# Optimization experiments

Measured on AMD Instinct MI355X. Metric: run time of the kernel, lower is better.

The kernel has to match this reference:

```python
import jax, jax.numpy as jnp
import numpy as np

B, S, D = 1, 2048, 2048
H = 16
HD = D // H           # 128
FFN_H = 5632          # int(2*4*D/3) rounded up to multiple of 256
EPS = 1e-5
ROPE_THETA = 10000.0


def rms_norm(x, w, eps=EPS):
    # x * rsqrt(mean(x^2, -1) + eps) * w
    return x * jax.lax.rsqrt(jnp.mean(x * x, axis=-1, keepdims=True) + eps) * w


def apply_rope(x, cos, sin):
    # x: [B, S, H, HD]; cos/sin: [S, HD//2]
    b, s, h, hd = x.shape
    xr = x.reshape(b, s, h, hd // 2, 2)
    x_re, x_im = xr[..., 0], xr[..., 1]
    c = cos[None, :, None, :]
    sn = sin[None, :, None, :]
    o_re = x_re * c - x_im * sn
    o_im = x_re * sn + x_im * c
    return jnp.stack([o_re, o_im], axis=-1).reshape(b, s, h, hd)


def setup_inputs() -> dict:
    key = jax.random.key(0)
    ks = jax.random.split(key, 10)
    x = jax.random.normal(ks[0], (B, S, D), dtype=jnp.float32)
    # RoPE frequencies (Llama-style)
    inv_freq = 1.0 / (ROPE_THETA ** (np.arange(0, HD, 2, dtype=np.float32) / HD))
    angles = np.outer(np.arange(S, dtype=np.float32), inv_freq)  # [S, HD//2]
    freqs_cos = jnp.asarray(np.cos(angles), dtype=jnp.float32)
    freqs_sin = jnp.asarray(np.sin(angles), dtype=jnp.float32)
    # causal mask: 1 = keep, 0 = masked
    mask = jnp.tril(jnp.ones((S, S), dtype=jnp.int32))[None, None]
    sc = 0.02
    return {
        "x": x,
        "freqs_cos": freqs_cos,
        "freqs_sin": freqs_sin,
        "mask": mask,
        "wq": jax.random.normal(ks[1], (D, D), jnp.float32) * sc,
        "wk": jax.random.normal(ks[2], (D, D), jnp.float32) * sc,
        "wv": jax.random.normal(ks[3], (D, D), jnp.float32) * sc,
        "wo": jax.random.normal(ks[4], (D, D), jnp.float32) * sc,
        "w1": jax.random.normal(ks[5], (D, FFN_H), jnp.float32) * sc,
        "w2": jax.random.normal(ks[6], (FFN_H, D), jnp.float32) * sc,
        "w3": jax.random.normal(ks[7], (D, FFN_H), jnp.float32) * sc,
        "attn_norm_w": jnp.ones((D,), jnp.float32),
        "ffn_norm_w": jnp.ones((D,), jnp.float32),
    }


def reference(x, freqs_cos, freqs_sin, mask, wq, wk, wv, wo, w1, w2, w3,
              attn_norm_w, ffn_norm_w):
    b, s, d = x.shape
    # --- attention block ---
    xn = rms_norm(x, attn_norm_w)
    q = (xn @ wq).reshape(b, s, H, HD)
    k = (xn @ wk).reshape(b, s, H, HD)
    v = (xn @ wv).reshape(b, s, H, HD)
    q = apply_rope(q, freqs_cos, freqs_sin)
    k = apply_rope(k, freqs_cos, freqs_sin)
    scores = jnp.einsum('bqhd,bkhd->bhqk', q, k) / jnp.sqrt(jnp.float32(HD))
    scores = jnp.where(mask == 0, -jnp.inf, scores)
    probs = jax.nn.softmax(scores, axis=-1)
    attn = jnp.einsum('bhqk,bkhd->bqhd', probs, v).reshape(b, s, d)
    h = x + attn @ wo
    # --- SwiGLU FFN block ---
    hn = rms_norm(h, ffn_norm_w)
    ff = (jax.nn.silu(hn @ w1) * (hn @ w3)) @ w2
    return h + ff
```

## Files before the change

### kernel.cpp

```cpp
#include <hip/hip_runtime.h>
#include <hip/hip_bf16.h>

typedef __bf16 bf16x8 __attribute__((ext_vector_type(8)));
typedef float f32x4 __attribute__((ext_vector_type(4)));
typedef unsigned short u16x8 __attribute__((ext_vector_type(8)));
typedef unsigned short u16x4 __attribute__((ext_vector_type(4)));

#define DEV static __device__ __forceinline__

DEV unsigned short f2bf(float f) {
    unsigned u = __builtin_bit_cast(unsigned, f);
    u += 0x7fffu + ((u >> 16) & 1u);
    return (unsigned short)(u >> 16);
}
DEV float bf2f(unsigned short h) {
    unsigned u = ((unsigned)h) << 16;
    return __builtin_bit_cast(float, u);
}

DEV void gl2lds16(const void* g, void* l) {
    __builtin_amdgcn_global_load_lds(
        (const __attribute__((address_space(1))) void*)g,
        (__attribute__((address_space(3))) void*)l, 16, 0, 0);
}

#define STAGE256(KT, SLOT, BUF)                                               \
    {                                                                         \
        const unsigned short* sbase = ((SLOT) & 1)                            \
            ? BT + (size_t)(bn + ((SLOT) >> 1) * 128) * K                     \
            : A  + (size_t)(bm + ((SLOT) >> 1) * 128) * K;                    \
        _Pragma("unroll")                                                     \
        for (int j = 0; j < 2; ++j) {                                         \
            const unsigned short* g = sbase + (size_t)(srow + j * 64) * K     \
                                      + (KT) * 64 + lc;                       \
            gl2lds16(g, &lds[BUF][SLOT][wave * 512 + j * 4096]);              \
        }                                                                     \
    }

#define COMPUTE256(BUF, MH, NH)                                               \
    {                                                                         \
        const char* Ab = (const char*)&lds[BUF][(MH) * 2][0];                 \
        const char* Bb = (const char*)&lds[BUF][(NH) * 2 + 1][0];             \
        bf16x8 a_[4][2], b_[2][2];                                            \
        _Pragma("unroll")                                                     \
        for (int m4 = 0; m4 < 4; ++m4) {                                      \
            _Pragma("unroll")                                                 \
            for (int kk = 0; kk < 2; ++kk)                                    \
                a_[m4][kk] = *(const bf16x8*)(Ab +                            \
                    (wm * 64 + m4 * 16 + lr) * 128 +                          \
                    ((kk * 64 + lg * 16) ^ xsw));                             \
        }                                                                     \
        _Pragma("unroll")                                                     \
        for (int n2 = 0; n2 < 2; ++n2) {                                      \
            _Pragma("unroll")                                                 \
            for (int kk = 0; kk < 2; ++kk)                                    \
                b_[n2][kk] = *(const bf16x8*)(Bb +                            \
                    (wn * 32 + n2 * 16 + lr) * 128 +                          \
                    ((kk * 64 + lg * 16) ^ xsw));                             \
        }                                                                     \
        __builtin_amdgcn_s_setprio(1);                                        \
        _Pragma("unroll")                                                     \
        for (int m4 = 0; m4 < 4; ++m4)                                        \
            _Pragma("unroll")                                                 \
            for (int n2 = 0; n2 < 2; ++n2)                                    \
                _Pragma("unroll")                                             \
                for (int kk = 0; kk < 2; ++kk)                                \
                    acc[(MH) * 4 + m4][(NH) * 2 + n2] =                       \
                        __builtin_amdgcn_mfma_f32_16x16x32_bf16(              \
                            a_[m4][kk], b_[n2][kk],                           \
                            acc[(MH) * 4 + m4][(NH) * 2 + n2], 0, 0, 0);      \
        __builtin_amdgcn_s_setprio(0);                                        \
    }

#define WAITV(N) asm volatile("s_waitcnt vmcnt(" #N ")" ::: "memory")
#define SBAR()   asm volatile("s_barrier" ::: "memory")

__global__ __launch_bounds__(512, 2)
void gemm256_bt(const unsigned short* __restrict__ A,
                const unsigned short* __restrict__ BT,
                unsigned short* __restrict__ outB,
                int M, int N, int K)
{
    __shared__ alignas(16) unsigned short lds[2][4][8192];

    const int tid  = threadIdx.x;
    const int lane = tid & 63;
    const int wave = tid >> 6;
    const int wm = wave >> 2;
    const int wn = wave & 3;
    const int lr = lane & 15;
    const int lg = lane >> 4;
    const int bm = blockIdx.y * 256;
    const int bn = blockIdx.x * 256;
    const int xsw  = (lr & 7) << 4;
    const int srow = tid >> 3;
    const int lc   = ((tid & 7) ^ (srow & 7)) * 8;

    f32x4 acc[8][4] = {};

    const int NT = K >> 6;

    STAGE256(0, 0, 0); STAGE256(0, 1, 0); STAGE256(0, 2, 0); STAGE256(0, 3, 0);

    for (int kt = 0; kt < NT - 1; ++kt) {
        const int buf = kt & 1, nbuf = buf ^ 1;
        STAGE256(kt + 1, 0, nbuf);
        WAITV(6); SBAR();
        COMPUTE256(buf, 0, 0);
        STAGE256(kt + 1, 1, nbuf);
        WAITV(6); SBAR();
        COMPUTE256(buf, 1, 0);
        STAGE256(kt + 1, 2, nbuf);
        WAITV(6); SBAR();
        COMPUTE256(buf, 1, 1);
        STAGE256(kt + 1, 3, nbuf);
        COMPUTE256(buf, 0, 1);
        SBAR();
    }
    {
        const int buf = (NT - 1) & 1;
        WAITV(4); SBAR();
        COMPUTE256(buf, 0, 0);
        WAITV(2); SBAR();
        COMPUTE256(buf, 1, 0);
        WAITV(0); SBAR();
        COMPUTE256(buf, 1, 1);
        COMPUTE256(buf, 0, 1);
    }

#pragma unroll
    for (int m = 0; m < 8; ++m) {
        const int row = bm + (m >> 2) * 128 + wm * 64 + (m & 3) * 16 + lg * 4;
#pragma unroll
        for (int n = 0; n < 4; ++n) {
            const int col = bn + (n >> 1) * 128 + wn * 32 + (n & 1) * 16 + lr;
#pragma unroll
            for (int r = 0; r < 4; ++r)
                outB[(size_t)(row + r) * N + col] = f2bf(acc[m][n][r]);
        }
    }
}

template <int EPI, int BM>
__global__ __launch_bounds__(256)
void gemm_bt(const unsigned short* __restrict__ A,
             const unsigned short* __restrict__ BT,
             unsigned short* __restrict__ outB,
             float* __restrict__ outF,
             const float* __restrict__ res,
             int M, int N, int K)
{
    constexpr int AM = BM / 32;
    constexpr int CAW = BM / 64;
    __shared__ alignas(16) unsigned short As[BM][32];
    __shared__ alignas(16) unsigned short Bs[128][32];

    const int tid  = threadIdx.x;
    const int lane = tid & 63;
    const int wave = tid >> 6;
    const int bm = blockIdx.y * BM;
    const int bn = blockIdx.x * 128;
    const int wm = (wave >> 1) * (BM / 2);
    const int wn = (wave & 1) * 64;
    const int lr = lane & 15;
    const int lg = lane >> 4;
    const int sub = lane >> 2;
    const int cb  = (lane & 3) * 16;

    f32x4 acc[AM][4] = {};

    auto stage = [&](int kt) {
#pragma unroll
        for (int ch = 0; ch < CAW; ++ch) {
            const int rb = wave * (CAW * 16) + ch * 16;
            const void* g = (const char*)(A + (size_t)(bm + rb + sub) * K + kt * 32) + cb;
            gl2lds16(g, &As[rb][0]);
        }
#pragma unroll
        for (int ch = 0; ch < 2; ++ch) {
            const int rb = wave * 32 + ch * 16;
            const void* g = (const char*)(BT + (size_t)(bn + rb + sub) * K + kt * 32) + cb;
            gl2lds16(g, &Bs[rb][0]);
        }
    };

    const int NT = K >> 5;
    for (int kt = 0; kt < NT; ++kt) {
        stage(kt);
        __syncthreads();
        bf16x8 af[AM], bfr[4];
#pragma unroll
        for (int i = 0; i < AM; ++i)
            af[i] = *reinterpret_cast<const bf16x8*>(&As[wm + i * 16 + lr][lg * 8]);
#pragma unroll
        for (int j = 0; j < 4; ++j)
            bfr[j] = *reinterpret_cast<const bf16x8*>(&Bs[wn + j * 16 + lr][lg * 8]);
#pragma unroll
        for (int i = 0; i < AM; ++i)
#pragma unroll
            for (int j = 0; j < 4; ++j)
                acc[i][j] = __builtin_amdgcn_mfma_f32_16x16x32_bf16(af[i], bfr[j], acc[i][j], 0, 0, 0);
        __syncthreads();
    }

#pragma unroll
    for (int i = 0; i < AM; ++i) {
#pragma unroll
        for (int j = 0; j < 4; ++j) {
            const int col = bn + wn + j * 16 + lr;
#pragma unroll
            for (int r = 0; r < 4; ++r) {
                const int row = bm + wm + i * 16 + lg * 4 + r;
                const float v = acc[i][j][r];
                if constexpr (EPI == 0) {
                    outB[(size_t)row * N + col] = f2bf(v);
                } else {
                    outF[(size_t)row * N + col] = res[(size_t)row * N + col] + v;
                }
            }
        }
    }
}

__global__ __launch_bounds__(256)
void rmsnorm_kernel(const float* __restrict__ x, const float* __restrict__ w,
                    unsigned short* __restrict__ out)
{
    const int row = blockIdx.x;
    const int tid = threadIdx.x;
    const float* xr = x + (size_t)row * 2048;
    const float4 a = *reinterpret_cast<const float4*>(xr + tid * 8);
    const float4 b = *reinterpret_cast<const float4*>(xr + tid * 8 + 4);
    float ss = a.x * a.x + a.y * a.y + a.z * a.z + a.w * a.w
             + b.x * b.x + b.y * b.y + b.z * b.z + b.w * b.w;
#pragma unroll
    for (int off = 32; off; off >>= 1) ss += __shfl_xor(ss, off);
    __shared__ float red[4];
    if ((tid & 63) == 0) red[tid >> 6] = ss;
    __syncthreads();
    const float tot = red[0] + red[1] + red[2] + red[3];
    const float sc = rsqrtf(tot * (1.0f / 2048.0f) + 1e-5f);
    const float4 wa = *reinterpret_cast<const float4*>(w + tid * 8);
    const float4 wb = *reinterpret_cast<const float4*>(w + tid * 8 + 4);
    u16x8 o;
    o[0] = f2bf(a.x * sc * wa.x); o[1] = f2bf(a.y * sc * wa.y);
    o[2] = f2bf(a.z * sc * wa.z); o[3] = f2bf(a.w * sc * wa.w);
    o[4] = f2bf(b.x * sc * wb.x); o[5] = f2bf(b.y * sc * wb.y);
    o[6] = f2bf(b.z * sc * wb.z); o[7] = f2bf(b.w * sc * wb.w);
    *reinterpret_cast<u16x8*>(out + (size_t)row * 2048 + tid * 8) = o;
}

__global__ __launch_bounds__(256)
void rope_kernel(unsigned short* __restrict__ t, const float* __restrict__ cs,
                 const float* __restrict__ sn)
{
    const int idx = blockIdx.x * 256 + threadIdx.x;
    const int s   = idx >> 9;
    const int col = (idx & 511) * 8;
    const int i0  = (col & 127) >> 1;
    u16x8 v = *reinterpret_cast<const u16x8*>(t + (size_t)s * 6144 + col);
    const float4 c  = *reinterpret_cast<const float4*>(cs + s * 64 + i0);
    const float4 sv = *reinterpret_cast<const float4*>(sn + s * 64 + i0);
    const float cc[4] = {c.x, c.y, c.z, c.w};
    const float ns[4] = {sv.x, sv.y, sv.z, sv.w};
#pragma unroll
    for (int p = 0; p < 4; ++p) {
        const float re = bf2f(v[2 * p]), im = bf2f(v[2 * p + 1]);
        v[2 * p]     = f2bf(re * cc[p] - im * ns[p]);
        v[2 * p + 1] = f2bf(re * ns[p] + im * cc[p]);
    }
    *reinterpret_cast<u16x8*>(t + (size_t)s * 6144 + col) = v;
}

__global__ __launch_bounds__(256)
void transpose_bf16(const unsigned short* __restrict__ in,
                    unsigned short* __restrict__ out, int M, int N, int ldin)
{
    __shared__ unsigned short t[64][66];
    const int bm = blockIdx.y * 64, bn = blockIdx.x * 64;
    const int tid = threadIdx.x;
    const int r = tid >> 3, c8 = (tid & 7) * 8;
#pragma unroll
    for (int i = 0; i < 2; ++i) {
        const int row = r + i * 32;
        u16x8 v = *reinterpret_cast<const u16x8*>(in + (size_t)(bm + row) * ldin + bn + c8);
#pragma unroll
        for (int e = 0; e < 8; ++e) t[row][c8 + e] = v[e];
    }
    __syncthreads();
#pragma unroll
    for (int i = 0; i < 2; ++i) {
        const int orow = r + i * 32;
        u16x8 v;
#pragma unroll
        for (int e = 0; e < 8; ++e) v[e] = t[c8 + e][orow];
        *reinterpret_cast<u16x8*>(out + (size_t)(bn + orow) * M + bm + c8) = v;
    }
}

__global__ __launch_bounds__(256)
void convT_kernel(const float* __restrict__ w, unsigned short* __restrict__ wT,
                  int K, int N)
{
    __shared__ unsigned short t[64][66];
    const int bk = blockIdx.y * 64, bn = blockIdx.x * 64;
    const int tid = threadIdx.x;
    const int r = tid >> 4, c4 = (tid & 15) * 4;
#pragma unroll
    for (int i = 0; i < 4; ++i) {
        const int row = r + i * 16;
        const float4 v = *reinterpret_cast<const float4*>(w + (size_t)(bk + row) * N + bn + c4);
        t[row][c4 + 0] = f2bf(v.x); t[row][c4 + 1] = f2bf(v.y);
        t[row][c4 + 2] = f2bf(v.z); t[row][c4 + 3] = f2bf(v.w);
    }
    __syncthreads();
#pragma unroll
    for (int i = 0; i < 4; ++i) {
        const int n = r + i * 16;
        u16x4 o;
#pragma unroll
        for (int e = 0; e < 4; ++e) o[e] = t[c4 + e][n];
        *reinterpret_cast<u16x4*>(wT + (size_t)(bn + n) * K + bk + c4) = o;
    }
}

__global__ __launch_bounds__(256)
void silu_mul_kernel(const unsigned short* __restrict__ t13,
                     unsigned short* __restrict__ g)
{
    const int s  = blockIdx.y;
    const int c8 = (blockIdx.x * 256 + threadIdx.x) * 8;
    if (c8 >= 5632) return;
    const unsigned short* row = t13 + (size_t)s * 11264;
    const u16x8 va = *reinterpret_cast<const u16x8*>(row + c8);
    const u16x8 vb = *reinterpret_cast<const u16x8*>(row + 5632 + c8);
    u16x8 o;
#pragma unroll
    for (int e = 0; e < 8; ++e) {
        const float x = bf2f(va[e]);
        const float y = bf2f(vb[e]);
        const float sv = x / (1.0f + __expf(-x));
        o[e] = f2bf(sv * y);
    }
    *reinterpret_cast<u16x8*>(g + (size_t)s * 5632 + c8) = o;
}

__global__ __launch_bounds__(512)
void flash_attn(const unsigned short* __restrict__ q,
                const unsigned short* __restrict__ k,
                const unsigned short* __restrict__ vT,
                unsigned short* __restrict__ attn)
{
    __shared__ alignas(16) unsigned short Ks[2][64][136];
    __shared__ alignas(16) unsigned short Vs[2][128][72];
    __shared__ alignas(16) unsigned short Ps[8][16][72];

    const int hh = blockIdx.y;
    const int pi = blockIdx.x;
    const int tid = threadIdx.x;
    const int lane = tid & 63, wave = tid >> 6;
    const int qt = (wave >> 2) ? (31 - pi) : pi;
    const int lr = lane & 15, lg = lane >> 4;
    const int q0 = qt * 64 + (wave & 3) * 16;
    const int myNT = qt + 1;
    const int NT   = 32 - pi;

    const int kr0 = tid >> 4, kc0 = (tid & 15) * 8;
    const int vr0 = tid >> 3, vc0 = (tid & 7) * 8;

    bf16x8 qf[4];
#pragma unroll
    for (int c = 0; c < 4; ++c)
        qf[c] = *reinterpret_cast<const bf16x8*>(
            q + (size_t)(q0 + lr) * 6144 + hh * 128 + c * 32 + lg * 8);

    f32x4 oacc[8] = {};
    float m_r[4], l_r[4];
#pragma unroll
    for (int r = 0; r < 4; ++r) { m_r[r] = -INFINITY; l_r[r] = 0.0f; }
    const float scale = 0.08838834764831845f;

    u16x8 kreg0, kreg1, vreg0, vreg1;
    auto gload = [&](int kt) {
        const int kv0 = kt * 64;
        kreg0 = *reinterpret_cast<const u16x8*>(k + (size_t)(kv0 + kr0) * 6144 + hh * 128 + kc0);
        kreg1 = *reinterpret_cast<const u16x8*>(k + (size_t)(kv0 + kr0 + 32) * 6144 + hh * 128 + kc0);
        vreg0 = *reinterpret_cast<const u16x8*>(vT + (size_t)(hh * 128 + vr0) * 2048 + kv0 + vc0);
        vreg1 = *reinterpret_cast<const u16x8*>(vT + (size_t)(hh * 128 + vr0 + 64) * 2048 + kv0 + vc0);
    };
    auto lwrite = [&](int buf) {
        *reinterpret_cast<u16x8*>(&Ks[buf][kr0][kc0])      = kreg0;
        *reinterpret_cast<u16x8*>(&Ks[buf][kr0 + 32][kc0]) = kreg1;
        *reinterpret_cast<u16x8*>(&Vs[buf][vr0][vc0])      = vreg0;
        *reinterpret_cast<u16x8*>(&Vs[buf][vr0 + 64][vc0]) = vreg1;
    };

    gload(0); lwrite(0);
    __syncthreads();

    for (int kt = 0; kt < NT; ++kt) {
        const int buf = kt & 1;
        if (kt + 1 < NT) gload(kt + 1);

        if (kt < myNT) {
            const int kv0 = kt * 64;
            const bool masked = (kt == myNT - 1);
            f32x4 s[4] = {};
            __builtin_amdgcn_s_setprio(1);
#pragma unroll
            for (int ct = 0; ct < 4; ++ct)
#pragma unroll
                for (int c = 0; c < 4; ++c) {
                    const bf16x8 kf = *reinterpret_cast<const bf16x8*>(
                        &Ks[buf][ct * 16 + lr][c * 32 + lg * 8]);
                    s[ct] = __builtin_amdgcn_mfma_f32_16x16x32_bf16(qf[c], kf, s[ct], 0, 0, 0);
                }
            __builtin_amdgcn_s_setprio(0);
#pragma unroll
            for (int ct = 0; ct < 4; ++ct)
#pragma unroll
                for (int r = 0; r < 4; ++r) {
                    float v = s[ct][r] * scale;
                    if (masked) {
                        const int kvg = kv0 + ct * 16 + lr;
                        const int qg  = q0 + lg * 4 + r;
                        if (kvg > qg) v = -INFINITY;
                    }
                    s[ct][r] = v;
                }
            float mn[4], alpha[4], rs[4];
#pragma unroll
            for (int r = 0; r < 4; ++r) {
                float v = fmaxf(fmaxf(s[0][r], s[1][r]), fmaxf(s[2][r], s[3][r]));
                v = fmaxf(v, __shfl_xor(v, 1));
                v = fmaxf(v, __shfl_xor(v, 2));
                v = fmaxf(v, __shfl_xor(v, 4));
                v = fmaxf(v, __shfl_xor(v, 8));
                mn[r] = fmaxf(m_r[r], v);
                alpha[r] = __expf(m_r[r] - mn[r]);
                m_r[r] = mn[r];
                rs[r] = 0.0f;
            }
#pragma unroll
            for (int ct = 0; ct < 4; ++ct)
#pragma unroll
                for (int r = 0; r < 4; ++r) {
                    const float p = __expf(s[ct][r] - mn[r]);
                    s[ct][r] = p;
                    rs[r] += p;
                }
#pragma unroll
            for (int r = 0; r < 4; ++r) {
                float t2 = rs[r];
                t2 += __shfl_xor(t2, 1);
                t2 += __shfl_xor(t2, 2);
                t2 += __shfl_xor(t2, 4);
                t2 += __shfl_xor(t2, 8);
                l_r[r] = l_r[r] * alpha[r] + t2;
            }
#pragma unroll
            for (int ot = 0; ot < 8; ++ot)
#pragma unroll
                for (int r = 0; r < 4; ++r) oacc[ot][r] *= alpha[r];

#pragma unroll
            for (int ct = 0; ct < 4; ++ct)
#pragma unroll
                for (int r = 0; r < 4; ++r)
                    Ps[wave][lg * 4 + r][ct * 16 + lr] = f2bf(s[ct][r]);

            __builtin_amdgcn_s_setprio(1);
#pragma unroll
            for (int c2 = 0; c2 < 2; ++c2) {
                const bf16x8 pf = *reinterpret_cast<const bf16x8*>(
                    &Ps[wave][lr][c2 * 32 + lg * 8]);
#pragma unroll
                for (int ot = 0; ot < 8; ++ot) {
                    const bf16x8 vf = *reinterpret_cast<const bf16x8*>(
                        &Vs[buf][ot * 16 + lr][c2 * 32 + lg * 8]);
                    oacc[ot] = __builtin_amdgcn_mfma_f32_16x16x32_bf16(pf, vf, oacc[ot], 0, 0, 0);
                }
            }
            __builtin_amdgcn_s_setprio(0);
        }

        if (kt + 1 < NT) lwrite(buf ^ 1);
        __syncthreads();
    }

#pragma unroll
    for (int ot = 0; ot < 8; ++ot)
#pragma unroll
        for (int r = 0; r < 4; ++r) {
            const float v = oacc[ot][r] / l_r[r];
            attn[(size_t)(q0 + lg * 4 + r) * 2048 + hh * 128 + ot * 16 + lr] = f2bf(v);
        }
}

extern "C" void kernel_launch(void* const* d_in, const int* in_sizes, int n_in,
                              void* d_out, int out_size, void* d_ws, size_t ws_size,
                              hipStream_t stream)
{
    const float* x    = (const float*)d_in[0];
    const float* fcos = (const float*)d_in[1];
    const float* fsin = (const float*)d_in[2];
    const float* wq  = (const float*)d_in[4];
    const float* wk  = (const float*)d_in[5];
    const float* wv  = (const float*)d_in[6];
    const float* wo  = (const float*)d_in[7];
    const float* w1  = (const float*)d_in[8];
    const float* w2  = (const float*)d_in[9];
    const float* w3  = (const float*)d_in[10];
    const float* anw = (const float*)d_in[11];
    const float* fnw = (const float*)d_in[12];
    float* out = (float*)d_out;

    char* ws = (char*)d_ws;
    size_t off = 0;
    auto alloc = [&](size_t bytes) { void* p = ws + off; off += bytes; return p; };
    const size_t SZ_DD = (size_t)2048 * 2048 * 2;
    const size_t SZ_DF = (size_t)2048 * 5632 * 2;

    unsigned short* wqT = (unsigned short*)alloc(SZ_DD);
    unsigned short* wkT = (unsigned short*)alloc(SZ_DD);
    unsigned short* wvT = (unsigned short*)alloc(SZ_DD);
    unsigned short* woT = (unsigned short*)alloc(SZ_DD);
    unsigned short* w1T = (unsigned short*)alloc(SZ_DF);
    unsigned short* w3T = (unsigned short*)alloc(SZ_DF);
    unsigned short* w2T = (unsigned short*)alloc(SZ_DF);

    char* reg1 = (char*)alloc((size_t)48 * 1024 * 1024);
    unsigned short* xn   = (unsigned short*)reg1;
    unsigned short* qkv  = (unsigned short*)(reg1 + SZ_DD);
    unsigned short* vTb  = (unsigned short*)(reg1 + SZ_DD + 3 * SZ_DD);
    unsigned short* ab   = (unsigned short*)(reg1 + SZ_DD + 4 * SZ_DD);
    unsigned short* t13  = (unsigned short*)reg1;

    char* reg2 = (char*)alloc(SZ_DF);
    unsigned short* hn = (unsigned short*)reg2;
    unsigned short* t1 = (unsigned short*)reg2;

    convT_kernel<<<dim3(32, 32), 256, 0, stream>>>(wq, wqT, 2048, 2048);
    convT_kernel<<<dim3(32, 32), 256, 0, stream>>>(wk, wkT, 2048, 2048);
    convT_kernel<<<dim3(32, 32), 256, 0, stream>>>(wv, wvT, 2048, 2048);
    convT_kernel<<<dim3(32, 32), 256, 0, stream>>>(wo, woT, 2048, 2048);
    convT_kernel<<<dim3(88, 32), 256, 0, stream>>>(w1, w1T, 2048, 5632);
    convT_kernel<<<dim3(88, 32), 256, 0, stream>>>(w3, w3T, 2048, 5632);
    convT_kernel<<<dim3(32, 88), 256, 0, stream>>>(w2, w2T, 5632, 2048);

    rmsnorm_kernel<<<2048, 256, 0, stream>>>(x, anw, xn);
    gemm256_bt<<<dim3(24, 8), 512, 0, stream>>>(xn, wqT, qkv, 2048, 6144, 2048);
    rope_kernel<<<4096, 256, 0, stream>>>(qkv, fcos, fsin);
    transpose_bf16<<<dim3(32, 32), 256, 0, stream>>>(qkv + 4096, vTb, 2048, 2048, 6144);
    flash_attn<<<dim3(16, 16), 512, 0, stream>>>(qkv, qkv + 2048, vTb, ab);
    gemm_bt<1, 64><<<dim3(16, 32), 256, 0, stream>>>(ab, woT, nullptr, out, x, 2048, 2048, 2048);

    rmsnorm_kernel<<<2048, 256, 0, stream>>>(out, fnw, hn);
    gemm256_bt<<<dim3(44, 8), 512, 0, stream>>>(hn, w1T, t13, 2048, 11264, 2048);
    silu_mul_kernel<<<dim3(3, 2048), 256, 0, stream>>>(t13, t1);
    gemm_bt<1, 64><<<dim3(16, 32), 256, 0, stream>>>(t1, w2T, nullptr, out, out, 2048, 2048, 5632);
}
```

Before: 488.3 us.

## Use pipelined 256-tile split-K GEMM for output projections and swizzle tile order

The simple 64x128 GEMM used for the wo and w2 projections is replaced by the double-buffered 256x256 GEMM, split over K into two halves. Each half writes fp32 partials, and a separate kernel sums them with the residual. All 256-tile GEMMs also remap block indices so that consecutive blocks share column tiles, which is meant to improve L2 reuse. The cost is extra fp32 partial traffic and a reduce launch. The split-K grid is only 128 blocks, which may underfill the GPU.

Measured after the change: 474.5 us. -2.8%, faster.

```diff
diff --git a/kernel.cpp b/kernel.cpp
--- a/kernel.cpp
+++ b/kernel.cpp
@@ -32,7 +32,7 @@
         _Pragma("unroll")                                                     \
         for (int j = 0; j < 2; ++j) {                                         \
             const unsigned short* g = sbase + (size_t)(srow + j * 64) * K     \
-                                      + (KT) * 64 + lc;                       \
+                                      + koff + (KT) * 64 + lc;                \
             gl2lds16(g, &lds[BUF][SLOT][wave * 512 + j * 4096]);              \
         }                                                                     \
     }
@@ -75,6 +75,51 @@
 #define WAITV(N) asm volatile("s_waitcnt vmcnt(" #N ")" ::: "memory")
 #define SBAR()   asm volatile("s_barrier" ::: "memory")
 
+#define GEMM256_PREAMBLE                                                      \
+    const int tid  = threadIdx.x;                                             \
+    const int lane = tid & 63;                                                \
+    const int wave = tid >> 6;                                                \
+    const int wm = wave >> 2;                                                 \
+    const int wn = wave & 3;                                                  \
+    const int lr = lane & 15;                                                 \
+    const int lg = lane >> 4;                                                 \
+    const int lin = blockIdx.y * gridDim.x + blockIdx.x;                      \
+    const int cpx = (gridDim.x * gridDim.y) >> 3;                             \
+    const int swz = (lin & 7) * cpx + (lin >> 3);                             \
+    const int bm = (swz & 7) * 256;            \
+    const int bn = (swz >> 3) * 256;                                          \
+    const int xsw  = (lr & 7) << 4;                                           \
+    const int srow = tid >> 3;                                                \
+    const int lc   = ((tid & 7) ^ (srow & 7)) * 8;
+
+#define GEMM256_MAINLOOP                                                      \
+    STAGE256(0, 0, 0); STAGE256(0, 1, 0); STAGE256(0, 2, 0); STAGE256(0, 3, 0);\
+    for (int kt = 0; kt < NT - 1; ++kt) {                                     \
+        const int buf = kt & 1, nbuf = buf ^ 1;                               \
+        STAGE256(kt + 1, 0, nbuf);                                            \
+        WAITV(6); SBAR();                                                     \
+        COMPUTE256(buf, 0, 0);                                                \
+        STAGE256(kt + 1, 1, nbuf);                                            \
+        WAITV(6); SBAR();                                                     \
+        COMPUTE256(buf, 1, 0);                                                \
+        STAGE256(kt + 1, 2, nbuf);                                            \
+        WAITV(6); SBAR();                                                     \
+        COMPUTE256(buf, 1, 1);                                                \
+        STAGE256(kt + 1, 3, nbuf);                                            \
+        COMPUTE256(buf, 0, 1);                                                \
+        SBAR();                                                               \
+    }                                                                         \
+    {                                                                         \
+        const int buf = (NT - 1) & 1;                                         \
+        WAITV(4); SBAR();                                                     \
+        COMPUTE256(buf, 0, 0);                                                \
+        WAITV(2); SBAR();                                                     \
+        COMPUTE256(buf, 1, 0);                                                \
+        WAITV(0); SBAR();                                                     \
+        COMPUTE256(buf, 1, 1);                                                \
+        COMPUTE256(buf, 0, 1);                                                \
+    }
+
 __global__ __launch_bounds__(512, 2)
 void gemm256_bt(const unsigned short* __restrict__ A,
                 const unsigned short* __restrict__ BT,
@@ -82,51 +127,12 @@
                 int M, int N, int K)
 {
     __shared__ alignas(16) unsigned short lds[2][4][8192];
-
-    const int tid  = threadIdx.x;
-    const int lane = tid & 63;
-    const int wave = tid >> 6;
-    const int wm = wave >> 2;
-    const int wn = wave & 3;
-    const int lr = lane & 15;
-    const int lg = lane >> 4;
-    const int bm = blockIdx.y * 256;
-    const int bn = blockIdx.x * 256;
-    const int xsw  = (lr & 7) << 4;
-    const int srow = tid >> 3;
-    const int lc   = ((tid & 7) ^ (srow & 7)) * 8;
-
+    GEMM256_PREAMBLE
+    const int koff = 0;
     f32x4 acc[8][4] = {};
-
     const int NT = K >> 6;
 
-    STAGE256(0, 0, 0); STAGE256(0, 1, 0); STAGE256(0, 2, 0); STAGE256(0, 3, 0);
-
-    for (int kt = 0; kt < NT - 1; ++kt) {
-        const int buf = kt & 1, nbuf = buf ^ 1;
-        STAGE256(kt + 1, 0, nbuf);
-        WAITV(6); SBAR();
-        COMPUTE256(buf, 0, 0);
-        STAGE256(kt + 1, 1, nbuf);
-        WAITV(6); SBAR();
-        COMPUTE256(buf, 1, 0);
-        STAGE256(kt + 1, 2, nbuf);
-        WAITV(6); SBAR();
-        COMPUTE256(buf, 1, 1);
-        STAGE256(kt + 1, 3, nbuf);
-        COMPUTE256(buf, 0, 1);
-        SBAR();
-    }
-    {
-        const int buf = (NT - 1) & 1;
-        WAITV(4); SBAR();
-        COMPUTE256(buf, 0, 0);
-        WAITV(2); SBAR();
-        COMPUTE256(buf, 1, 0);
-        WAITV(0); SBAR();
-        COMPUTE256(buf, 1, 1);
-        COMPUTE256(buf, 0, 1);
-    }
+    GEMM256_MAINLOOP
 
 #pragma unroll
     for (int m = 0; m < 8; ++m) {
@@ -141,84 +147,46 @@
     }
 }
 
-template <int EPI, int BM>
+__global__ __launch_bounds__(512, 2)
+void gemm256_splitk(const unsigned short* __restrict__ A,
+                    const unsigned short* __restrict__ BT,
+                    float* __restrict__ outP,
+                    int M, int N, int K)
+{
+    __shared__ alignas(16) unsigned short lds[2][4][8192];
+    GEMM256_PREAMBLE
+    const int Kh = K >> 1;
+    const int koff = blockIdx.z * Kh;
+    f32x4 acc[8][4] = {};
+    const int NT = Kh >> 6;
+
+    GEMM256_MAINLOOP
+
+    float* P = outP + (size_t)blockIdx.z * M * N;
+#pragma unroll
+    for (int m = 0; m < 8; ++m) {
+        const int row = bm + (m >> 2) * 128 + wm * 64 + (m & 3) * 16 + lg * 4;
+#pragma unroll
+        for (int n = 0; n < 4; ++n) {
+            const int col = bn + (n >> 1) * 128 + wn * 32 + (n & 1) * 16 + lr;
+#pragma unroll
+            for (int r = 0; r < 4; ++r)
+                P[(size_t)(row + r) * N + col] = acc[m][n][r];
+        }
+    }
+}
+
 __global__ __launch_bounds__(256)
-void gemm_bt(const unsigned short* __restrict__ A,
-             const unsigned short* __restrict__ BT,
-             unsigned short* __restrict__ outB,
-             float* __restrict__ outF,
-             const float* __restrict__ res,
-             int M, int N, int K)
-{
-    constexpr int AM = BM / 32;
-    constexpr int CAW = BM / 64;
-    __shared__ alignas(16) unsigned short As[BM][32];
-    __shared__ alignas(16) unsigned short Bs[128][32];
-
-    const int tid  = threadIdx.x;
-    const int lane = tid & 63;
-    const int wave = tid >> 6;
-    const int bm = blockIdx.y * BM;
-    const int bn = blockIdx.x * 128;
-    const int wm = (wave >> 1) * (BM / 2);
-    const int wn = (wave & 1) * 64;
-    const int lr = lane & 15;
-    const int lg = lane >> 4;
-    const int sub = lane >> 2;
-    const int cb  = (lane & 3) * 16;
-
-    f32x4 acc[AM][4] = {};
-
-    auto stage = [&](int kt) {
-#pragma unroll
-        for (int ch = 0; ch < CAW; ++ch) {
-            const int rb = wave * (CAW * 16) + ch * 16;
-            const void* g = (const char*)(A + (size_t)(bm + rb + sub) * K + kt * 32) + cb;
-            gl2lds16(g, &As[rb][0]);
-        }
-#pragma unroll
-        for (int ch = 0; ch < 2; ++ch) {
-            const int rb = wave * 32 + ch * 16;
-            const void* g = (const char*)(BT + (size_t)(bn + rb + sub) * K + kt * 32) + cb;
-            gl2lds16(g, &Bs[rb][0]);
-        }
-    };
-
-    const int NT = K >> 5;
-    for (int kt = 0; kt < NT; ++kt) {
-        stage(kt);
-        __syncthreads();
-        bf16x8 af[AM], bfr[4];
-#pragma unroll
-        for (int i = 0; i < AM; ++i)
-            af[i] = *reinterpret_cast<const bf16x8*>(&As[wm + i * 16 + lr][lg * 8]);
-#pragma unroll
-        for (int j = 0; j < 4; ++j)
-            bfr[j] = *reinterpret_cast<const bf16x8*>(&Bs[wn + j * 16 + lr][lg * 8]);
-#pragma unroll
-        for (int i = 0; i < AM; ++i)
-#pragma unroll
-            for (int j = 0; j < 4; ++j)
-                acc[i][j] = __builtin_amdgcn_mfma_f32_16x16x32_bf16(af[i], bfr[j], acc[i][j], 0, 0, 0);
-        __syncthreads();
-    }
-
-#pragma unroll
-    for (int i = 0; i < AM; ++i) {
-#pragma unroll
-        for (int j = 0; j < 4; ++j) {
-            const int col = bn + wn + j * 16 + lr;
-#pragma unroll
-            for (int r = 0; r < 4; ++r) {
-                const int row = bm + wm + i * 16 + lg * 4 + r;
-                const float v = acc[i][j][r];
-                if constexpr (EPI == 0) {
-                    outB[(size_t)row * N + col] = f2bf(v);
-                } else {
-                    outF[(size_t)row * N + col] = res[(size_t)row * N + col] + v;
-                }
-            }
-        }
+void reduce2_add(const float* res, const float* p, float* out, int n4)
+{
+    const float4* r4 = (const float4*)res;
+    const float4* a4 = (const float4*)p;
+    const float4* b4 = (const float4*)(p + (size_t)2048 * 2048);
+    float4* o4 = (float4*)out;
+    for (int i = blockIdx.x * 256 + threadIdx.x; i < n4; i += gridDim.x * 256) {
+        const float4 r = r4[i], a = a4[i], b = b4[i];
+        o4[i] = make_float4(r.x + a.x + b.x, r.y + a.y + b.y,
+                            r.z + a.z + b.z, r.w + a.w + b.w);
     }
 }
 
@@ -535,10 +503,13 @@
     unsigned short* vTb  = (unsigned short*)(reg1 + SZ_DD + 3 * SZ_DD);
     unsigned short* ab   = (unsigned short*)(reg1 + SZ_DD + 4 * SZ_DD);
     unsigned short* t13  = (unsigned short*)reg1;
+    float*          pk   = (float*)reg1;
 
     char* reg2 = (char*)alloc(SZ_DF);
     unsigned short* hn = (unsigned short*)reg2;
     unsigned short* t1 = (unsigned short*)reg2;
+
+    const int N4 = 2048 * 2048 / 4;
 
     convT_kernel<<<dim3(32, 32), 256, 0, stream>>>(wq, wqT, 2048, 2048);
     convT_kernel<<<dim3(32, 32), 256, 0, stream>>>(wk, wkT, 2048, 2048);
@@ -553,10 +524,12 @@
     rope_kernel<<<4096, 256, 0, stream>>>(qkv, fcos, fsin);
     transpose_bf16<<<dim3(32, 32), 256, 0, stream>>>(qkv + 4096, vTb, 2048, 2048, 6144);
     flash_attn<<<dim3(16, 16), 512, 0, stream>>>(qkv, qkv + 2048, vTb, ab);
-    gemm_bt<1, 64><<<dim3(16, 32), 256, 0, stream>>>(ab, woT, nullptr, out, x, 2048, 2048, 2048);
+    gemm256_splitk<<<dim3(8, 8, 2), 512, 0, stream>>>(ab, woT, pk, 2048, 2048, 2048);
+    reduce2_add<<<2048, 256, 0, stream>>>(x, pk, out, N4);
 
     rmsnorm_kernel<<<2048, 256, 0, stream>>>(out, fnw, hn);
     gemm256_bt<<<dim3(44, 8), 512, 0, stream>>>(hn, w1T, t13, 2048, 11264, 2048);
     silu_mul_kernel<<<dim3(3, 2048), 256, 0, stream>>>(t13, t1);
-    gemm_bt<1, 64><<<dim3(16, 32), 256, 0, stream>>>(t1, w2T, nullptr, out, out, 2048, 2048, 5632);
-}
+    gemm256_splitk<<<dim3(8, 8, 2), 512, 0, stream>>>(t1, w2T, pk, 2048, 2048, 5632);
+    reduce2_add<<<2048, 256, 0, stream>>>(out, pk, out, N4);
+}
```

## Replace small GEMMs with split-K 128x256 kernel, fuse reduce with RMSNorm, swizzle blocks

Applied to the files above, without the earlier changes.

Drops the simple single-buffered gemm_bt kernel and adds a double-buffered 128x256 LDS-staged GEMM. The Wo and W2 projections use it in split-K form (two halves written as fp32 partials), followed by a reduction kernel. For Wo, the reduction also adds the residual and performs the FFN RMSNorm, which removes a separate norm pass. The W1/W3 GEMM moves to the 128-row tile to get more blocks. Block-index swizzling is added to both GEMMs for L2 locality. In exchange, the split-K path writes and re-reads fp32 partial buffers through global memory.

Result: faster. 450.6 us (-7.7%).

```diff
diff --git a/kernel.cpp b/kernel.cpp
--- a/kernel.cpp
+++ b/kernel.cpp
@@ -23,6 +23,9 @@
         (const __attribute__((address_space(1))) void*)g,
         (__attribute__((address_space(3))) void*)l, 16, 0, 0);
 }
+
+#define WAITV(N) asm volatile("s_waitcnt vmcnt(" #N ")" ::: "memory")
+#define SBAR()   asm volatile("s_barrier" ::: "memory")
 
 #define STAGE256(KT, SLOT, BUF)                                               \
     {                                                                         \
@@ -72,9 +75,6 @@
         __builtin_amdgcn_s_setprio(0);                                        \
     }
 
-#define WAITV(N) asm volatile("s_waitcnt vmcnt(" #N ")" ::: "memory")
-#define SBAR()   asm volatile("s_barrier" ::: "memory")
-
 __global__ __launch_bounds__(512, 2)
 void gemm256_bt(const unsigned short* __restrict__ A,
                 const unsigned short* __restrict__ BT,
@@ -82,7 +82,6 @@
                 int M, int N, int K)
 {
     __shared__ alignas(16) unsigned short lds[2][4][8192];
-
     const int tid  = threadIdx.x;
     const int lane = tid & 63;
     const int wave = tid >> 6;
@@ -90,18 +89,19 @@
     const int wn = wave & 3;
     const int lr = lane & 15;
     const int lg = lane >> 4;
-    const int bm = blockIdx.y * 256;
-    const int bn = blockIdx.x * 256;
+    const int lin = blockIdx.y * gridDim.x + blockIdx.x;
+    const int cpx = (gridDim.x * gridDim.y) >> 3;
+    const int swz = (lin & 7) * cpx + (lin >> 3);
+    const int bm = (swz & 7) * 256;
+    const int bn = (swz >> 3) * 256;
     const int xsw  = (lr & 7) << 4;
     const int srow = tid >> 3;
     const int lc   = ((tid & 7) ^ (srow & 7)) * 8;
 
     f32x4 acc[8][4] = {};
-
     const int NT = K >> 6;
 
     STAGE256(0, 0, 0); STAGE256(0, 1, 0); STAGE256(0, 2, 0); STAGE256(0, 3, 0);
-
     for (int kt = 0; kt < NT - 1; ++kt) {
         const int buf = kt & 1, nbuf = buf ^ 1;
         STAGE256(kt + 1, 0, nbuf);
@@ -141,84 +141,159 @@
     }
 }
 
-template <int EPI, int BM>
-__global__ __launch_bounds__(256)
-void gemm_bt(const unsigned short* __restrict__ A,
-             const unsigned short* __restrict__ BT,
-             unsigned short* __restrict__ outB,
-             float* __restrict__ outF,
-             const float* __restrict__ res,
-             int M, int N, int K)
-{
-    constexpr int AM = BM / 32;
-    constexpr int CAW = BM / 64;
-    __shared__ alignas(16) unsigned short As[BM][32];
-    __shared__ alignas(16) unsigned short Bs[128][32];
-
+#define STAGE128(KT, SLOT, BUF)                                               \
+    {                                                                         \
+        const unsigned short* sbase = ((SLOT) == 0)                           \
+            ? A  + (size_t)bm * K                                             \
+            : BT + (size_t)(bn + ((SLOT) - 1) * 128) * K;                     \
+        _Pragma("unroll")                                                     \
+        for (int j = 0; j < 2; ++j) {                                         \
+            const unsigned short* g = sbase + (size_t)(srow + j * 64) * K     \
+                                      + koff + (KT) * 64 + lc;                \
+            gl2lds16(g, &lds[BUF][SLOT][wave * 512 + j * 4096]);              \
+        }                                                                     \
+    }
+
+#define COMPUTE128(BUF, KK)                                                   \
+    {                                                                         \
+        const char* Ab = (const char*)&lds[BUF][0][0];                        \
+        const char* Bb = (const char*)&lds[BUF][1 + (wn >> 1)][0];            \
+        bf16x8 a_[4], b_[4];                                                  \
+        _Pragma("unroll")                                                     \
+        for (int m4 = 0; m4 < 4; ++m4)                                        \
+            a_[m4] = *(const bf16x8*)(Ab + (wm * 64 + m4 * 16 + lr) * 128 +   \
+                     (((KK) * 64 + lg * 16) ^ xsw));                          \
+        _Pragma("unroll")                                                     \
+        for (int n2 = 0; n2 < 4; ++n2)                                        \
+            b_[n2] = *(const bf16x8*)(Bb +                                    \
+                     ((wn & 1) * 64 + n2 * 16 + lr) * 128 +                   \
+                     (((KK) * 64 + lg * 16) ^ xsw));                          \
+        __builtin_amdgcn_s_setprio(1);                                        \
+        _Pragma("unroll")                                                     \
+        for (int m4 = 0; m4 < 4; ++m4)                                        \
+            _Pragma("unroll")                                                 \
+            for (int n2 = 0; n2 < 4; ++n2)                                    \
+                acc[m4][n2] = __builtin_amdgcn_mfma_f32_16x16x32_bf16(        \
+                    a_[m4], b_[n2], acc[m4][n2], 0, 0, 0);                    \
+        __builtin_amdgcn_s_setprio(0);                                        \
+    }
+
+template <bool SPLITK>
+__global__ __launch_bounds__(512, 2)
+void gemm128_bt(const unsigned short* __restrict__ A,
+                const unsigned short* __restrict__ BT,
+                unsigned short* __restrict__ outB,
+                float* __restrict__ outP,
+                int M, int N, int K)
+{
+    __shared__ alignas(16) unsigned short lds[2][3][8192];
     const int tid  = threadIdx.x;
     const int lane = tid & 63;
     const int wave = tid >> 6;
-    const int bm = blockIdx.y * BM;
-    const int bn = blockIdx.x * 128;
-    const int wm = (wave >> 1) * (BM / 2);
-    const int wn = (wave & 1) * 64;
+    const int wm = wave >> 2;
+    const int wn = wave & 3;
     const int lr = lane & 15;
     const int lg = lane >> 4;
-    const int sub = lane >> 2;
-    const int cb  = (lane & 3) * 16;
-
-    f32x4 acc[AM][4] = {};
-
-    auto stage = [&](int kt) {
-#pragma unroll
-        for (int ch = 0; ch < CAW; ++ch) {
-            const int rb = wave * (CAW * 16) + ch * 16;
-            const void* g = (const char*)(A + (size_t)(bm + rb + sub) * K + kt * 32) + cb;
-            gl2lds16(g, &As[rb][0]);
-        }
-#pragma unroll
-        for (int ch = 0; ch < 2; ++ch) {
-            const int rb = wave * 32 + ch * 16;
-            const void* g = (const char*)(BT + (size_t)(bn + rb + sub) * K + kt * 32) + cb;
-            gl2lds16(g, &Bs[rb][0]);
-        }
-    };
-
-    const int NT = K >> 5;
-    for (int kt = 0; kt < NT; ++kt) {
-        stage(kt);
-        __syncthreads();
-        bf16x8 af[AM], bfr[4];
-#pragma unroll
-        for (int i = 0; i < AM; ++i)
-            af[i] = *reinterpret_cast<const bf16x8*>(&As[wm + i * 16 + lr][lg * 8]);
-#pragma unroll
-        for (int j = 0; j < 4; ++j)
-            bfr[j] = *reinterpret_cast<const bf16x8*>(&Bs[wn + j * 16 + lr][lg * 8]);
-#pragma unroll
-        for (int i = 0; i < AM; ++i)
-#pragma unroll
-            for (int j = 0; j < 4; ++j)
-                acc[i][j] = __builtin_amdgcn_mfma_f32_16x16x32_bf16(af[i], bfr[j], acc[i][j], 0, 0, 0);
-        __syncthreads();
-    }
-
-#pragma unroll
-    for (int i = 0; i < AM; ++i) {
-#pragma unroll
-        for (int j = 0; j < 4; ++j) {
-            const int col = bn + wn + j * 16 + lr;
+    const int gy  = gridDim.y;
+    const int lin = blockIdx.y * gridDim.x + blockIdx.x;
+    const int cpx = (gridDim.x * gy) >> 3;
+    const int swz = (lin & 7) * cpx + (lin >> 3);
+    const int bm = (swz % gy) * 128;
+    const int bn = (swz / gy) * 256;
+    const int xsw  = (lr & 7) << 4;
+    const int srow = tid >> 3;
+    const int lc   = ((tid & 7) ^ (srow & 7)) * 8;
+    int koff, NT;
+    if constexpr (SPLITK) { const int Kh = K >> 1; koff = blockIdx.z * Kh; NT = Kh >> 6; }
+    else                  { koff = 0;              NT = K >> 6; }
+
+    f32x4 acc[4][4] = {};
+
+    STAGE128(0, 0, 0); STAGE128(0, 1, 0); STAGE128(0, 2, 0);
+    for (int kt = 0; kt < NT - 1; ++kt) {
+        const int buf = kt & 1, nbuf = buf ^ 1;
+        STAGE128(kt + 1, 0, nbuf);
+        STAGE128(kt + 1, 1, nbuf);
+        WAITV(4); SBAR();
+        COMPUTE128(buf, 0);
+        STAGE128(kt + 1, 2, nbuf);
+        COMPUTE128(buf, 1);
+        SBAR();
+    }
+    {
+        const int buf = (NT - 1) & 1;
+        WAITV(0); SBAR();
+        COMPUTE128(buf, 0);
+        COMPUTE128(buf, 1);
+    }
+
+#pragma unroll
+    for (int m4 = 0; m4 < 4; ++m4) {
+        const int row = bm + wm * 64 + m4 * 16 + lg * 4;
+#pragma unroll
+        for (int n2 = 0; n2 < 4; ++n2) {
+            const int col = bn + wn * 64 + n2 * 16 + lr;
 #pragma unroll
             for (int r = 0; r < 4; ++r) {
-                const int row = bm + wm + i * 16 + lg * 4 + r;
-                const float v = acc[i][j][r];
-                if constexpr (EPI == 0) {
-                    outB[(size_t)row * N + col] = f2bf(v);
-                } else {
-                    outF[(size_t)row * N + col] = res[(size_t)row * N + col] + v;
-                }
+                if constexpr (SPLITK)
+                    outP[(size_t)blockIdx.z * M * N + (size_t)(row + r) * N + col] = acc[m4][n2][r];
+                else
+                    outB[(size_t)(row + r) * N + col] = f2bf(acc[m4][n2][r]);
             }
         }
+    }
+}
+
+__global__ __launch_bounds__(256)
+void reduce2_add(const float* res, const float* p, float* out, int n4)
+{
+    const float4* r4 = (const float4*)res;
+    const float4* a4 = (const float4*)p;
+    const float4* b4 = (const float4*)(p + (size_t)2048 * 2048);
+    float4* o4 = (float4*)out;
+    for (int i = blockIdx.x * 256 + threadIdx.x; i < n4; i += gridDim.x * 256) {
+        const float4 r = r4[i], a = a4[i], b = b4[i];
+        o4[i] = make_float4(r.x + a.x + b.x, r.y + a.y + b.y,
+                            r.z + a.z + b.z, r.w + a.w + b.w);
+    }
+}
+
+__global__ __launch_bounds__(256)
+void reduce2_norm(const float* __restrict__ res, const float* __restrict__ p,
+                  const float* __restrict__ w, float* __restrict__ hout,
+                  unsigned short* __restrict__ nout)
+{
+    const int row = blockIdx.x, tid = threadIdx.x;
+    const float4* r4 = (const float4*)(res + (size_t)row * 2048);
+    const float4* a4 = (const float4*)(p   + (size_t)row * 2048);
+    const float4* b4 = (const float4*)(p + (size_t)2048 * 2048 + (size_t)row * 2048);
+    float4* h4 = (float4*)(hout + (size_t)row * 2048);
+    float4 h[2];
+    float ss = 0.f;
+#pragma unroll
+    for (int i = 0; i < 2; ++i) {
+        const int idx = i * 256 + tid;
+        const float4 r = r4[idx], a = a4[idx], b = b4[idx];
+        float4 v = make_float4(r.x + a.x + b.x, r.y + a.y + b.y,
+                               r.z + a.z + b.z, r.w + a.w + b.w);
+        h[i] = v; h4[idx] = v;
+        ss += v.x * v.x + v.y * v.y + v.z * v.z + v.w * v.w;
+    }
+#pragma unroll
+    for (int off = 32; off; off >>= 1) ss += __shfl_xor(ss, off);
+    __shared__ float red[4];
+    if ((tid & 63) == 0) red[tid >> 6] = ss;
+    __syncthreads();
+    const float tot = red[0] + red[1] + red[2] + red[3];
+    const float sc = rsqrtf(tot * (1.0f / 2048.0f) + 1e-5f);
+#pragma unroll
+    for (int i = 0; i < 2; ++i) {
+        const int idx = i * 256 + tid;
+        const float4 wv = ((const float4*)w)[idx];
+        u16x4 o;
+        o[0] = f2bf(h[i].x * sc * wv.x); o[1] = f2bf(h[i].y * sc * wv.y);
+        o[2] = f2bf(h[i].z * sc * wv.z); o[3] = f2bf(h[i].w * sc * wv.w);
+        *(u16x4*)(nout + (size_t)row * 2048 + idx * 4) = o;
     }
 }
 
@@ -535,10 +610,13 @@
     unsigned short* vTb  = (unsigned short*)(reg1 + SZ_DD + 3 * SZ_DD);
     unsigned short* ab   = (unsigned short*)(reg1 + SZ_DD + 4 * SZ_DD);
     unsigned short* t13  = (unsigned short*)reg1;
+    float*          pk   = (float*)reg1;
 
     char* reg2 = (char*)alloc(SZ_DF);
     unsigned short* hn = (unsigned short*)reg2;
     unsigned short* t1 = (unsigned short*)reg2;
+
+    const int N4 = 2048 * 2048 / 4;
 
     convT_kernel<<<dim3(32, 32), 256, 0, stream>>>(wq, wqT, 2048, 2048);
     convT_kernel<<<dim3(32, 32), 256, 0, stream>>>(wk, wkT, 2048, 2048);
@@ -553,10 +631,11 @@
     rope_kernel<<<4096, 256, 0, stream>>>(qkv, fcos, fsin);
     transpose_bf16<<<dim3(32, 32), 256, 0, stream>>>(qkv + 4096, vTb, 2048, 2048, 6144);
     flash_attn<<<dim3(16, 16), 512, 0, stream>>>(qkv, qkv + 2048, vTb, ab);
-    gemm_bt<1, 64><<<dim3(16, 32), 256, 0, stream>>>(ab, woT, nullptr, out, x, 2048, 2048, 2048);
-
-    rmsnorm_kernel<<<2048, 256, 0, stream>>>(out, fnw, hn);
-    gemm256_bt<<<dim3(44, 8), 512, 0, stream>>>(hn, w1T, t13, 2048, 11264, 2048);
+    gemm128_bt<true><<<dim3(8, 16, 2), 512, 0, stream>>>(ab, woT, nullptr, pk, 2048, 2048, 2048);
+    reduce2_norm<<<2048, 256, 0, stream>>>(x, pk, fnw, out, hn);
+
+    gemm128_bt<false><<<dim3(44, 16), 512, 0, stream>>>(hn, w1T, t13, nullptr, 2048, 11264, 2048);
     silu_mul_kernel<<<dim3(3, 2048), 256, 0, stream>>>(t13, t1);
-    gemm_bt<1, 64><<<dim3(16, 32), 256, 0, stream>>>(t1, w2T, nullptr, out, out, 2048, 2048, 5632);
-}
+    gemm128_bt<true><<<dim3(8, 16, 2), 512, 0, stream>>>(t1, w2T, nullptr, pk, 2048, 2048, 5632);
+    reduce2_add<<<2048, 256, 0, stream>>>(out, pk, out, N4);
+}
```
